# Kernel tuning notes

Hardware: AMD Instinct MI355X
Metric: run time of the kernel (lower is better)

## Reference

```python
import jax, jax.numpy as jnp
import numpy as np

B, T, E, H = 4, 2048, 1024, 16
HS = E // H
FF = 4 * E


def _layernorm(x, g, b, eps=1e-5):
    mu = jnp.mean(x, axis=-1, keepdims=True)
    var = jnp.var(x, axis=-1, keepdims=True)
    return (x - mu) * jax.lax.rsqrt(var + eps) * g + b


def setup_inputs() -> dict:
    key = jax.random.key(0)
    ks = jax.random.split(key, 12)
    s = E ** -0.5
    return {
        "x": jax.random.normal(ks[0], (B, T, E), jnp.float32),
        "Wq": jax.random.normal(ks[1], (E, E), jnp.float32) * s,
        "Wk": jax.random.normal(ks[2], (E, E), jnp.float32) * s,
        "Wv": jax.random.normal(ks[3], (E, E), jnp.float32) * s,
        "Wp": jax.random.normal(ks[4], (E, E), jnp.float32) * s,
        "bp": jnp.zeros((E,), jnp.float32),
        "W1": jax.random.normal(ks[5], (E, FF), jnp.float32) * s,
        "b1": jnp.zeros((FF,), jnp.float32),
        "W2": jax.random.normal(ks[6], (FF, E), jnp.float32) * (FF ** -0.5),
        "b2": jnp.zeros((E,), jnp.float32),
        "g1": jnp.ones((E,), jnp.float32),
        "be1": jnp.zeros((E,), jnp.float32),
        "g2": jnp.ones((E,), jnp.float32),
        "be2": jnp.zeros((E,), jnp.float32),
    }


def reference(x, Wq, Wk, Wv, Wp, bp, W1, b1, W2, b2, g1, be1, g2, be2):
    h = _layernorm(x, g1, be1)
    # per-head projections: Wq columns laid out head-by-head (matches concat order)
    q = (h @ Wq).reshape(B, T, H, HS).transpose(0, 2, 1, 3)  # [B,H,T,hs]
    k = (h @ Wk).reshape(B, T, H, HS).transpose(0, 2, 1, 3)
    v = (h @ Wv).reshape(B, T, H, HS).transpose(0, 2, 1, 3)
    # NOTE: original scales by full embedding size C**-0.5, not head_size
    scores = jnp.einsum("bhqd,bhkd->bhqk", q, k) * (E ** -0.5)
    causal = jnp.tril(jnp.ones((T, T), bool))
    scores = jnp.where(causal, scores, -jnp.inf)
    wei = jax.nn.softmax(scores, axis=-1)
    attn = jnp.einsum("bhqk,bhkd->bhqd", wei, v)  # [B,H,T,hs]
    attn = attn.transpose(0, 2, 1, 3).reshape(B, T, E)
    x = x + attn @ Wp + bp
    h2 = _layernorm(x, g2, be2)
    ff = jax.nn.relu(h2 @ W1 + b1) @ W2 + b2
    return x + ff
```

## Files before the change

kernel.cpp:

```cpp
#include <hip/hip_runtime.h>
#include <stdint.h>

typedef unsigned short u16;
typedef short s8v __attribute__((ext_vector_type(8)));
typedef float f32x4 __attribute__((ext_vector_type(4)));

#define B_SZ 4
#define T_SEQ 2048
#define E_DIM 1024
#define H_NUM 16
#define HS 64
#define FF_DIM 4096
#define M_ROWS 8192
#define QSCALE 0.0450842200f

__device__ __forceinline__ u16 f2bf(float f) {
    unsigned int u = __builtin_bit_cast(unsigned int, f);
    u += 0x7fffu + ((u >> 16) & 1u);
    return (u16)(u >> 16);
}

__device__ __forceinline__ float bf2f(u16 u) {
    unsigned int v = ((unsigned int)u) << 16;
    return __builtin_bit_cast(float, v);
}

__device__ __forceinline__ void async_copy16(const void* g, void* l) {
    __builtin_amdgcn_global_load_lds(
        (const __attribute__((address_space(1))) unsigned int*)g,
        (__attribute__((address_space(3))) unsigned int*)l, 16, 0, 0);
}

__global__ __launch_bounds__(256)
void transpose_cast4(const float* __restrict__ s0, const float* __restrict__ s1,
                     const float* __restrict__ s2, const float* __restrict__ s3,
                     u16* __restrict__ dqkv, u16* __restrict__ dp) {
    __shared__ float tile[32][33];
    const int zz = blockIdx.z;
    const float* src = (zz == 0) ? s0 : (zz == 1) ? s1 : (zz == 2) ? s2 : s3;
    u16* dst = (zz < 3) ? dqkv + (size_t)zz * 1048576 : dp;
    int n0 = blockIdx.x * 32, k0 = blockIdx.y * 32;
    int tx = threadIdx.x, ty = threadIdx.y;
#pragma unroll
    for (int i = 0; i < 4; i++)
        tile[ty + i * 8][tx] = src[(size_t)(k0 + ty + i * 8) * 1024 + n0 + tx];
    __syncthreads();
#pragma unroll
    for (int i = 0; i < 4; i++)
        dst[(size_t)(n0 + ty + i * 8) * 1024 + k0 + tx] = f2bf(tile[tx][ty + i * 8]);
}

__global__ __launch_bounds__(256)
void transpose_cast_w12(const float* __restrict__ W1, const float* __restrict__ W2,
                        u16* __restrict__ d1, u16* __restrict__ d2) {
    __shared__ float tile[32][33];
    const int zz = blockIdx.z;
    const float* src;
    u16* dst;
    int n0, k0, N, K;
    if (zz == 0) {
        src = W1; dst = d1; N = 4096; K = 1024;
        n0 = blockIdx.x * 32; k0 = blockIdx.y * 32;
    } else {
        src = W2; dst = d2; N = 1024; K = 4096;
        int idx = blockIdx.y * 128 + blockIdx.x;
        n0 = (idx & 31) * 32; k0 = (idx >> 5) * 32;
    }
    int tx = threadIdx.x, ty = threadIdx.y;
#pragma unroll
    for (int i = 0; i < 4; i++)
        tile[ty + i * 8][tx] = src[(size_t)(k0 + ty + i * 8) * N + n0 + tx];
    __syncthreads();
#pragma unroll
    for (int i = 0; i < 4; i++)
        dst[(size_t)(n0 + ty + i * 8) * K + k0 + tx] = f2bf(tile[tx][ty + i * 8]);
}

__global__ __launch_bounds__(256)
void transpose_v(const u16* __restrict__ V, u16* __restrict__ VT) {
    __shared__ u16 tile[64][80];
    const int t0 = blockIdx.x * 64;
    const size_t hoff = (size_t)blockIdx.y * (T_SEQ * HS);
    const int r = threadIdx.x >> 2, c0 = (threadIdx.x & 3) * 16;
    const u16* src = V + hoff + (size_t)(t0 + r) * HS + c0;
    *(s8v*)&tile[r][c0] = *(const s8v*)src;
    *(s8v*)&tile[r][c0 + 8] = *(const s8v*)(src + 8);
    __syncthreads();
    u16 tmp[16];
#pragma unroll
    for (int e = 0; e < 16; e++) tmp[e] = tile[c0 + e][r];
    u16* dst = VT + hoff + (size_t)r * T_SEQ + t0 + c0;
    *(s8v*)dst = *(const s8v*)&tmp[0];
    *(s8v*)(dst + 8) = *(const s8v*)&tmp[8];
}

__global__ __launch_bounds__(256)
void ln_kernel(const float* __restrict__ x, const float* __restrict__ g,
               const float* __restrict__ b, u16* __restrict__ out) {
    int row = blockIdx.x;
    int tid = threadIdx.x;
    float4 v = ((const float4*)(x + (size_t)row * E_DIM))[tid];
    float s = v.x + v.y + v.z + v.w;
    float sq = v.x * v.x + v.y * v.y + v.z * v.z + v.w * v.w;
#pragma unroll
    for (int off = 32; off; off >>= 1) {
        s += __shfl_xor(s, off);
        sq += __shfl_xor(sq, off);
    }
    __shared__ float sh[8];
    int w = tid >> 6, lane = tid & 63;
    if (lane == 0) { sh[w] = s; sh[4 + w] = sq; }
    __syncthreads();
    s = sh[0] + sh[1] + sh[2] + sh[3];
    sq = sh[4] + sh[5] + sh[6] + sh[7];
    float mu = s * (1.f / E_DIM);
    float var = sq * (1.f / E_DIM) - mu * mu;
    float rs = rsqrtf(var + 1e-5f);
    float4 gv = ((const float4*)g)[tid];
    float4 bv = ((const float4*)b)[tid];
    ushort4 o;
    o.x = f2bf((v.x - mu) * rs * gv.x + bv.x);
    o.y = f2bf((v.y - mu) * rs * gv.y + bv.y);
    o.z = f2bf((v.z - mu) * rs * gv.z + bv.z);
    o.w = f2bf((v.w - mu) * rs * gv.w + bv.w);
    ((ushort4*)(out + (size_t)row * E_DIM))[tid] = o;
}

__global__ __launch_bounds__(256)
void ln_kernel_bf(const u16* __restrict__ x, const float* __restrict__ g,
                  const float* __restrict__ b, u16* __restrict__ out) {
    int row = blockIdx.x;
    int tid = threadIdx.x;
    ushort4 uv = ((const ushort4*)(x + (size_t)row * E_DIM))[tid];
    float4 v;
    v.x = bf2f(uv.x); v.y = bf2f(uv.y); v.z = bf2f(uv.z); v.w = bf2f(uv.w);
    float s = v.x + v.y + v.z + v.w;
    float sq = v.x * v.x + v.y * v.y + v.z * v.z + v.w * v.w;
#pragma unroll
    for (int off = 32; off; off >>= 1) {
        s += __shfl_xor(s, off);
        sq += __shfl_xor(sq, off);
    }
    __shared__ float sh[8];
    int w = tid >> 6, lane = tid & 63;
    if (lane == 0) { sh[w] = s; sh[4 + w] = sq; }
    __syncthreads();
    s = sh[0] + sh[1] + sh[2] + sh[3];
    sq = sh[4] + sh[5] + sh[6] + sh[7];
    float mu = s * (1.f / E_DIM);
    float var = sq * (1.f / E_DIM) - mu * mu;
    float rs = rsqrtf(var + 1e-5f);
    float4 gv = ((const float4*)g)[tid];
    float4 bv = ((const float4*)b)[tid];
    ushort4 o;
    o.x = f2bf((v.x - mu) * rs * gv.x + bv.x);
    o.y = f2bf((v.y - mu) * rs * gv.y + bv.y);
    o.z = f2bf((v.z - mu) * rs * gv.z + bv.z);
    o.w = f2bf((v.w - mu) * rs * gv.w + bv.w);
    ((ushort4*)(out + (size_t)row * E_DIM))[tid] = o;
}

template <int MODE>
__global__ __launch_bounds__(512)
void gemm_bt128(const u16* __restrict__ A, const u16* __restrict__ BT,
                int M, int N, int K,
                const float* __restrict__ bias, const float* __restrict__ resid,
                float* __restrict__ outf, u16* __restrict__ outb) {
    __shared__ __align__(16) u16 As[3][256 * 64];
    __shared__ __align__(16) u16 Bs[3][128 * 64];

    const int gx = gridDim.x;
    const int nwg = gx * gridDim.y;
    const int l = blockIdx.y * gx + blockIdx.x;
    const int sw = (l & 7) * (nwg >> 3) + (l >> 3);
    const int tRow = (sw / gx) * 256, tCol = (sw % gx) * 128;

    const int tid = threadIdx.x, w = tid >> 6, lane = tid & 63;
    const int wr = w >> 1, wc = w & 1, lr = lane & 15, hg = lane >> 4;
    const int nk = K >> 6;

    f32x4 z = {0.f, 0.f, 0.f, 0.f};
    f32x4 acc[4][4];
#pragma unroll
    for (int m = 0; m < 4; m++)
#pragma unroll
        for (int n = 0; n < 4; n++) acc[m][n] = z;

    auto STAGE_A = [&](int kt, int c) {
#pragma unroll
        for (int i = 0; i < 4; i++) {
            int chunk = i * 512 + tid;
            int row = chunk >> 3, j = chunk & 7;
            int js = (j ^ (row & 7)) << 3;
            async_copy16(A + (size_t)(tRow + row) * K + (kt << 6) + js,
                         &As[c][(i * 512 + w * 64) * 8]);
        }
    };
    auto STAGE_B = [&](int kt, int c) {
#pragma unroll
        for (int i = 0; i < 2; i++) {
            int chunk = i * 512 + tid;
            int row = chunk >> 3, j = chunk & 7;
            int js = (j ^ (row & 7)) << 3;
            async_copy16(BT + (size_t)(tCol + row) * K + (kt << 6) + js,
                         &Bs[c][(i * 512 + w * 64) * 8]);
        }
    };

    STAGE_A(0, 0); STAGE_B(0, 0);
    STAGE_A(1, 1); STAGE_B(1, 1);
    asm volatile("s_waitcnt vmcnt(6)" ::: "memory");
    asm volatile("s_barrier" ::: "memory");

    for (int t = 0; t < nk; ++t) {
        const int bu = t % 3, nx = (t + 2) % 3;
        const u16* Ab = &As[bu][0];
        const u16* Bb = &Bs[bu][0];
        const bool more = (t + 2 < nk);

        s8v af0[2][2], bf[4][2];
#pragma unroll
        for (int m = 0; m < 2; m++)
#pragma unroll
            for (int kk = 0; kk < 2; kk++) {
                int r = wr * 64 + m * 16 + lr;
                af0[m][kk] = *(const s8v*)&Ab[r * 64 + (((kk * 4 + hg) ^ (r & 7)) << 3)];
            }
#pragma unroll
        for (int n = 0; n < 4; n++)
#pragma unroll
            for (int kk = 0; kk < 2; kk++) {
                int r = wc * 64 + n * 16 + lr;
                bf[n][kk] = *(const s8v*)&Bb[r * 64 + (((kk * 4 + hg) ^ (r & 7)) << 3)];
            }
        if (more) STAGE_A(t + 2, nx);
        asm volatile("s_barrier" ::: "memory");
        __builtin_amdgcn_s_setprio(1);
#pragma unroll
        for (int m = 0; m < 2; m++)
#pragma unroll
            for (int n = 0; n < 4; n++)
#pragma unroll
                for (int kk = 0; kk < 2; kk++)
                    acc[m][n] = __builtin_amdgcn_mfma_f32_16x16x32_bf16(
                        af0[m][kk], bf[n][kk], acc[m][n], 0, 0, 0);
        __builtin_amdgcn_s_setprio(0);
        asm volatile("s_barrier" ::: "memory");

        s8v af1[2][2];
#pragma unroll
        for (int m = 0; m < 2; m++)
#pragma unroll
            for (int kk = 0; kk < 2; kk++) {
                int r = wr * 64 + (m + 2) * 16 + lr;
                af1[m][kk] = *(const s8v*)&Ab[r * 64 + (((kk * 4 + hg) ^ (r & 7)) << 3)];
            }
        if (more) STAGE_B(t + 2, nx);
        asm volatile("s_barrier" ::: "memory");
        __builtin_amdgcn_s_setprio(1);
#pragma unroll
        for (int m = 0; m < 2; m++)
#pragma unroll
            for (int n = 0; n < 4; n++)
#pragma unroll
                for (int kk = 0; kk < 2; kk++)
                    acc[m + 2][n] = __builtin_amdgcn_mfma_f32_16x16x32_bf16(
                        af1[m][kk], bf[n][kk], acc[m + 2][n], 0, 0, 0);
        __builtin_amdgcn_s_setprio(0);
        if (more) asm volatile("s_waitcnt vmcnt(6)" ::: "memory");
        else      asm volatile("s_waitcnt vmcnt(0)" ::: "memory");
        asm volatile("s_barrier" ::: "memory");
    }

#pragma unroll
    for (int m = 0; m < 4; m++)
#pragma unroll
        for (int n = 0; n < 4; n++)
#pragma unroll
            for (int r = 0; r < 4; r++) {
                int row = tRow + wr * 64 + m * 16 + hg * 4 + r;
                int col = tCol + wc * 64 + n * 16 + lr;
                float v = acc[m][n][r];
                if (MODE == 0) {
                    int type = col >> 10, c2 = col & 1023;
                    int h = c2 >> 6, d = c2 & 63;
                    int bb = row >> 11, tt = row & 2047;
                    if (type == 0) v *= QSCALE;
                    outb[(size_t)type * 8388608 +
                         (((size_t)(bb * H_NUM + h) * T_SEQ + tt) << 6) + d] = f2bf(v);
                } else if (MODE == 1) {
                    v += bias[col];
                    v = fmaxf(v, 0.f);
                    outb[(size_t)row * N + col] = f2bf(v);
                } else {
                    outb[(size_t)row * N + col] =
                        f2bf(resid[(size_t)row * N + col] + v + bias[col]);
                }
            }
}

template <int MODE>
__global__ __launch_bounds__(512)
void gemm_bt256(const u16* __restrict__ A, const u16* __restrict__ BT,
                int M, int N, int Kst, int klen,
                const float* __restrict__ bias, const float* __restrict__ resid,
                float* __restrict__ outf, u16* __restrict__ outb) {
    __shared__ __align__(16) u16 As[2][256 * 64];
    __shared__ __align__(16) u16 Bs[2][256 * 64];

    const int gx = gridDim.x;
    const int nwg = gx * gridDim.y;
    const int l = blockIdx.y * gx + blockIdx.x;
    const int sw = (l & 7) * (nwg >> 3) + (l >> 3);
    const int tRow = (sw / gx) * 256, tCol = (sw % gx) * 256;
    const size_t koff = (size_t)blockIdx.z * klen;
    const u16* Az = A + koff;
    const u16* BTz = BT + koff;

    const int tid = threadIdx.x, w = tid >> 6, lane = tid & 63;
    const int wr = w >> 2, wc = w & 3, lr = lane & 15, hg = lane >> 4;
    const int nk = klen >> 6;

    f32x4 z = {0.f, 0.f, 0.f, 0.f};
    f32x4 acc[8][4];
#pragma unroll
    for (int m = 0; m < 8; m++)
#pragma unroll
        for (int n = 0; n < 4; n++) acc[m][n] = z;

    auto STAGE_A = [&](int kt, int c, int h) {
#pragma unroll
        for (int i = 0; i < 2; i++) {
            int chunk = h * 1024 + i * 512 + tid;
            int row = chunk >> 3, j = chunk & 7;
            int js = (j ^ (row & 7)) << 3;
            async_copy16(Az + (size_t)(tRow + row) * Kst + (kt << 6) + js,
                         &As[c][(h * 1024 + i * 512 + w * 64) * 8]);
        }
    };
    auto STAGE_B = [&](int kt, int c, int h) {
#pragma unroll
        for (int i = 0; i < 2; i++) {
            int chunk = h * 1024 + i * 512 + tid;
            int row = chunk >> 3, j = chunk & 7;
            int js = (j ^ (row & 7)) << 3;
            async_copy16(BTz + (size_t)(tCol + row) * Kst + (kt << 6) + js,
                         &Bs[c][(h * 1024 + i * 512 + w * 64) * 8]);
        }
    };

    STAGE_B(0, 0, 0); STAGE_B(0, 0, 1); STAGE_A(0, 0, 0); STAGE_A(0, 0, 1);
    STAGE_B(1, 1, 0); STAGE_B(1, 1, 1); STAGE_A(1, 1, 0); STAGE_A(1, 1, 1);
    asm volatile("s_waitcnt vmcnt(6)" ::: "memory");
    asm volatile("s_barrier" ::: "memory");

    for (int t = 0; t < nk; ++t) {
        const int cur = t & 1;
        const u16* Ab = &As[cur][0];
        const u16* Bb = &Bs[cur][0];
        const bool more = (t + 2 < nk);

        s8v bf[4][2];
#pragma unroll
        for (int p = 0; p < 4; p++) {
            s8v af[2][2];
#pragma unroll
            for (int mm = 0; mm < 2; mm++)
#pragma unroll
                for (int kk = 0; kk < 2; kk++) {
                    int r = (2 * p + mm) * 32 + wr * 16 + lr;
                    af[mm][kk] = *(const s8v*)&Ab[r * 64 + (((kk * 4 + hg) ^ (r & 7)) << 3)];
                }
            if (p == 0) {
#pragma unroll
                for (int n = 0; n < 4; n++)
#pragma unroll
                    for (int kk = 0; kk < 2; kk++) {
                        int r = n * 64 + wc * 16 + lr;
                        bf[n][kk] = *(const s8v*)&Bb[r * 64 + (((kk * 4 + hg) ^ (r & 7)) << 3)];
                    }
            }
            if (more) {
                if (p == 0) STAGE_B(t + 2, cur, 0);
                else if (p == 1) STAGE_B(t + 2, cur, 1);
                else if (p == 2) STAGE_A(t + 2, cur, 0);
                else STAGE_A(t + 2, cur, 1);
            }
            asm volatile("s_barrier" ::: "memory");
            __builtin_amdgcn_s_setprio(1);
#pragma unroll
            for (int mm = 0; mm < 2; mm++)
#pragma unroll
                for (int n = 0; n < 4; n++)
#pragma unroll
                    for (int kk = 0; kk < 2; kk++)
                        acc[2 * p + mm][n] = __builtin_amdgcn_mfma_f32_16x16x32_bf16(
                            af[mm][kk], bf[n][kk], acc[2 * p + mm][n], 0, 0, 0);
            __builtin_amdgcn_s_setprio(0);
            if (p == 3) {
                if (more) asm volatile("s_waitcnt vmcnt(6)" ::: "memory");
                else      asm volatile("s_waitcnt vmcnt(0)" ::: "memory");
            }
            asm volatile("s_barrier" ::: "memory");
        }
    }

    u16* outp = outb;
    if (MODE == 3 && blockIdx.z == 1) outp = (u16*)outf;
#pragma unroll
    for (int m = 0; m < 8; m++)
#pragma unroll
        for (int n = 0; n < 4; n++)
#pragma unroll
            for (int r = 0; r < 4; r++) {
                int row = tRow + m * 32 + wr * 16 + hg * 4 + r;
                int col = tCol + n * 64 + wc * 16 + lr;
                float v = acc[m][n][r];
                if (MODE == 1) {
                    v += bias[col];
                    v = fmaxf(v, 0.f);
                    outp[(size_t)row * N + col] = f2bf(v);
                } else {
                    outp[(size_t)row * N + col] = f2bf(v);
                }
            }
}

__global__ __launch_bounds__(256)
void reduce_w2(const u16* __restrict__ p0, const u16* __restrict__ p1,
               const u16* __restrict__ resid, const float* __restrict__ bias,
               float* __restrict__ out) {
    const int total = M_ROWS * E_DIM / 4;
    for (int i = blockIdx.x * 256 + threadIdx.x; i < total; i += gridDim.x * 256) {
        ushort4 rr = ((const ushort4*)resid)[i];
        float4 bb = ((const float4*)bias)[i & 255];
        ushort4 a = ((const ushort4*)p0)[i];
        ushort4 c = ((const ushort4*)p1)[i];
        float4 o;
        o.x = bf2f(a.x) + bf2f(c.x) + bf2f(rr.x) + bb.x;
        o.y = bf2f(a.y) + bf2f(c.y) + bf2f(rr.y) + bb.y;
        o.z = bf2f(a.z) + bf2f(c.z) + bf2f(rr.z) + bb.z;
        o.w = bf2f(a.w) + bf2f(c.w) + bf2f(rr.w) + bb.w;
        ((float4*)out)[i] = o;
    }
}

__global__ __launch_bounds__(512)
void attn_kernel(const u16* __restrict__ Q, const u16* __restrict__ K,
                 const u16* __restrict__ VT, u16* __restrict__ O) {
    __shared__ u16 Ks[2][64 * 64];
    __shared__ u16 Vs[2][64 * 64];
    __shared__ u16 Pl[8][16 * 64];
    const int bh = blockIdx.y;
    const u16* Qh = Q + (size_t)bh * T_SEQ * HS;
    const u16* Kh = K + (size_t)bh * T_SEQ * HS;
    const u16* VTh = VT + (size_t)bh * T_SEQ * HS;
    const int tid = threadIdx.x, w = tid >> 6, lane = tid & 63;
    const int lr = lane & 15, hg = lane >> 4;
    const int swz = (lr & 7) << 3;
    const int bb = bh >> 4, hh = bh & 15;
    const f32x4 z = {0.f, 0.f, 0.f, 0.f};

    for (int half = 0; half < 2; ++half) {
        const int qt = half ? (15 - blockIdx.x) : blockIdx.x;
        const int qb = qt * 128;
        const int nt = 2 * qt + 2;

        s8v qf[2];
        {
            const int qrow = qb + w * 16 + lr;
            qf[0] = *(const s8v*)(Qh + (size_t)qrow * HS + hg * 8);
            qf[1] = *(const s8v*)(Qh + (size_t)qrow * HS + 32 + hg * 8);
        }
        f32x4 o[4] = {z, z, z, z};
        float m_run[4] = {-1e30f, -1e30f, -1e30f, -1e30f};
        float l_part[4] = {0.f, 0.f, 0.f, 0.f};

        auto STAGE = [&](int t, int c) {
            int chunk = tid;
            int row = chunk >> 3, j = chunk & 7;
            int js = (j ^ (row & 7)) << 3;
            async_copy16(Kh + (size_t)t * (64 * HS) + row * HS + js, &Ks[c][w * 512]);
            async_copy16(VTh + (size_t)row * T_SEQ + t * 64 + js, &Vs[c][w * 512]);
        };

        int cur = 0;
        STAGE(0, 0);
        __syncthreads();

        for (int t = 0; t < nt; ++t) {
            if (t + 1 < nt) STAGE(t + 1, cur ^ 1);

            f32x4 s[4];
            __builtin_amdgcn_s_setprio(1);
#pragma unroll
            for (int n = 0; n < 4; n++) {
                f32x4 a = z;
#pragma unroll
                for (int kc = 0; kc < 2; kc++) {
                    s8v bfr = *(const s8v*)&Ks[cur][((n * 16 + lr) * 64 + kc * 32 + hg * 8) ^ swz];
                    a = __builtin_amdgcn_mfma_f32_16x16x32_bf16(qf[kc], bfr, a, 0, 0, 0);
                }
                s[n] = a;
            }
            __builtin_amdgcn_s_setprio(0);
            const bool diag = (t >= nt - 2);
            if (diag) {
#pragma unroll
                for (int n = 0; n < 4; n++)
#pragma unroll
                    for (int r = 0; r < 4; r++)
                        if ((t * 64 + n * 16 + lr) > (qb + w * 16 + hg * 4 + r))
                            s[n][r] = -1e30f;
            }
            float d0[4][4];
            float dm = -1e30f;
#pragma unroll
            for (int n = 0; n < 4; n++)
#pragma unroll
                for (int r = 0; r < 4; r++) {
                    d0[n][r] = s[n][r] - m_run[r];
                    dm = fmaxf(dm, d0[n][r]);
                }
            if (__any(dm > 8.f)) {
                float pm[4];
#pragma unroll
                for (int r = 0; r < 4; r++) {
                    float m0 = fmaxf(fmaxf(s[0][r], s[1][r]), fmaxf(s[2][r], s[3][r]));
                    m0 = fmaxf(m0, __shfl_xor(m0, 1));
                    m0 = fmaxf(m0, __shfl_xor(m0, 2));
                    m0 = fmaxf(m0, __shfl_xor(m0, 4));
                    m0 = fmaxf(m0, __shfl_xor(m0, 8));
                    pm[r] = m0;
                }
#pragma unroll
                for (int r = 0; r < 4; r++) {
                    float mn = fmaxf(m_run[r], pm[r]);
                    float al = __builtin_amdgcn_exp2f(m_run[r] - mn);
                    m_run[r] = mn;
                    l_part[r] *= al;
                    o[0][r] *= al; o[1][r] *= al; o[2][r] *= al; o[3][r] *= al;
                }
#pragma unroll
                for (int n = 0; n < 4; n++)
#pragma unroll
                    for (int r = 0; r < 4; r++) d0[n][r] = s[n][r] - m_run[r];
            }
#pragma unroll
            for (int n = 0; n < 4; n++)
#pragma unroll
                for (int r = 0; r < 4; r++) {
                    float p = __builtin_amdgcn_exp2f(d0[n][r]);
                    s[n][r] = p;
                    l_part[r] += p;
                }
            u16* Pw = &Pl[w][0];
#pragma unroll
            for (int n = 0; n < 4; n++)
#pragma unroll
                for (int r = 0; r < 4; r++) {
                    int prow = hg * 4 + r;
                    float pv = s[n][r];
                    Pw[(prow * 64 + n * 16 + lr) ^ ((prow & 7) << 3)] =
                        (u16)(__builtin_bit_cast(unsigned int, pv) >> 16);
                }
            asm volatile("s_waitcnt lgkmcnt(0)" ::: "memory");
            __builtin_amdgcn_s_setprio(1);
#pragma unroll
            for (int n = 0; n < 4; n++) {
#pragma unroll
                for (int kc = 0; kc < 2; kc++) {
                    s8v pa = *(const s8v*)&Pw[(lr * 64 + kc * 32 + hg * 8) ^ swz];
                    s8v vb = *(const s8v*)&Vs[cur][((n * 16 + lr) * 64 + kc * 32 + hg * 8) ^ swz];
                    o[n] = __builtin_amdgcn_mfma_f32_16x16x32_bf16(pa, vb, o[n], 0, 0, 0);
                }
            }
            __builtin_amdgcn_s_setprio(0);
            __syncthreads();
            cur ^= 1;
        }
        float rl[4];
#pragma unroll
        for (int r = 0; r < 4; r++) {
            float lsum = l_part[r];
            lsum += __shfl_xor(lsum, 1);
            lsum += __shfl_xor(lsum, 2);
            lsum += __shfl_xor(lsum, 4);
            lsum += __shfl_xor(lsum, 8);
            rl[r] = 1.f / lsum;
        }
#pragma unroll
        for (int n = 0; n < 4; n++)
#pragma unroll
            for (int r = 0; r < 4; r++) {
                int trow = qb + w * 16 + hg * 4 + r;
                O[((size_t)(bb * T_SEQ + trow)) * E_DIM + hh * HS + n * 16 + lr] =
                    f2bf(o[n][r] * rl[r]);
            }
    }
}

extern "C" void kernel_launch(void* const* d_in, const int* in_sizes, int n_in,
                              void* d_out, int out_size, void* d_ws, size_t ws_size,
                              hipStream_t stream) {
    (void)in_sizes; (void)n_in; (void)out_size; (void)ws_size;
    const float* x  = (const float*)d_in[0];
    const float* Wq = (const float*)d_in[1];
    const float* Wk = (const float*)d_in[2];
    const float* Wv = (const float*)d_in[3];
    const float* Wp = (const float*)d_in[4];
    const float* bp = (const float*)d_in[5];
    const float* W1 = (const float*)d_in[6];
    const float* b1 = (const float*)d_in[7];
    const float* W2 = (const float*)d_in[8];
    const float* b2 = (const float*)d_in[9];
    const float* g1  = (const float*)d_in[10];
    const float* be1 = (const float*)d_in[11];
    const float* g2  = (const float*)d_in[12];
    const float* be2 = (const float*)d_in[13];

    char* ws = (char*)d_ws;
    u16* wqkv_t  = (u16*)(ws);
    u16* wp_t    = (u16*)(ws + 6291456);
    u16* w1_t    = (u16*)(ws + 8388608);
    u16* w2_t    = (u16*)(ws + 16777216);
    u16* h_bf    = (u16*)(ws + 25165824);
    u16* q_bf    = (u16*)(ws + 41943040);
    u16* attn_bf = q_bf + 3 * 8388608;
    u16* ff1     = q_bf;
    u16* x2b     = (u16*)(ws + 109051904);
    u16* vt_bf   = h_bf;
    u16* part0   = (u16*)ws;
    u16* part1   = h_bf;

    dim3 b32(32, 8);
    transpose_cast4<<<dim3(32, 32, 4), b32, 0, stream>>>(Wq, Wk, Wv, Wp, wqkv_t, wp_t);
    transpose_cast_w12<<<dim3(128, 32, 2), b32, 0, stream>>>(W1, W2, w1_t, w2_t);

    ln_kernel<<<M_ROWS, 256, 0, stream>>>(x, g1, be1, h_bf);
    gemm_bt128<0><<<dim3(24, 32), 512, 0, stream>>>(h_bf, wqkv_t, M_ROWS, 3072, 1024,
                                                    nullptr, nullptr, nullptr, q_bf);
    transpose_v<<<dim3(32, 64), 256, 0, stream>>>(q_bf + 2 * 8388608, vt_bf);
    attn_kernel<<<dim3(8, 64), 512, 0, stream>>>(q_bf, q_bf + 8388608, vt_bf, attn_bf);
    gemm_bt128<2><<<dim3(8, 32), 512, 0, stream>>>(attn_bf, wp_t, M_ROWS, 1024, 1024,
                                                   bp, x, nullptr, x2b);
    ln_kernel_bf<<<M_ROWS, 256, 0, stream>>>(x2b, g2, be2, h_bf);
    gemm_bt256<1><<<dim3(16, 32), 512, 0, stream>>>(h_bf, w1_t, M_ROWS, 4096, 1024, 1024,
                                                    b1, nullptr, nullptr, ff1);
    gemm_bt256<3><<<dim3(4, 32, 2), 512, 0, stream>>>(ff1, w2_t, M_ROWS, 1024, 4096, 2048,
                                                      nullptr, nullptr, (float*)part1, part0);
    reduce_w2<<<2048, 256, 0, stream>>>(part0, part1, x2b, b2, (float*)d_out);
}
```

Before: 343.6 us.

## Software-pipeline LDS fragment reads with MFMA using double-buffered registers

Restructures the GEMM main loop so the A fragments for the next phase, and the A/B fragments for the next k-tile, are read from LDS while the current phase's MFMAs run. Two register sets alternate between phases, and the loop is unrolled by two so the B fragment buffers swap roles. This also removes one of the two barriers per phase. The goal is to hide LDS read latency behind matrix-core work and cut synchronisation, at the cost of more live registers. The unroll-by-two assumes an even tile count.

```diff
diff --git a/kernel.cpp b/kernel.cpp
--- a/kernel.cpp
+++ b/kernel.cpp
@@ -349,61 +349,83 @@
         }
     };
 
+    s8v afa[2][2], afb[2][2];
+    s8v bfa[4][2], bfb[4][2];
+
+    auto READ_A = [&](const u16* Ab, int p, s8v (&af)[2][2]) {
+#pragma unroll
+        for (int mm = 0; mm < 2; mm++)
+#pragma unroll
+            for (int kk = 0; kk < 2; kk++) {
+                int r = (2 * p + mm) * 32 + wr * 16 + lr;
+                af[mm][kk] = *(const s8v*)&Ab[r * 64 + (((kk * 4 + hg) ^ (r & 7)) << 3)];
+            }
+    };
+    auto READ_B = [&](const u16* Bb, s8v (&bf)[4][2]) {
+#pragma unroll
+        for (int n = 0; n < 4; n++)
+#pragma unroll
+            for (int kk = 0; kk < 2; kk++) {
+                int r = n * 64 + wc * 16 + lr;
+                bf[n][kk] = *(const s8v*)&Bb[r * 64 + (((kk * 4 + hg) ^ (r & 7)) << 3)];
+            }
+    };
+
     STAGE_B(0, 0, 0); STAGE_B(0, 0, 1); STAGE_A(0, 0, 0); STAGE_A(0, 0, 1);
     STAGE_B(1, 1, 0); STAGE_B(1, 1, 1); STAGE_A(1, 1, 0); STAGE_A(1, 1, 1);
     asm volatile("s_waitcnt vmcnt(6)" ::: "memory");
     asm volatile("s_barrier" ::: "memory");
-
-    for (int t = 0; t < nk; ++t) {
+    READ_A(&As[0][0], 0, afa);
+    READ_B(&Bs[0][0], bfa);
+
+#define MFMA8(AF, BF, R0)                                                      \
+    __builtin_amdgcn_s_setprio(1);                                             \
+    _Pragma("unroll") for (int mm = 0; mm < 2; mm++)                           \
+        _Pragma("unroll") for (int n = 0; n < 4; n++)                          \
+            _Pragma("unroll") for (int kk = 0; kk < 2; kk++)                   \
+                acc[R0 + mm][n] = __builtin_amdgcn_mfma_f32_16x16x32_bf16(     \
+                    AF[mm][kk], BF[n][kk], acc[R0 + mm][n], 0, 0, 0);          \
+    __builtin_amdgcn_s_setprio(0);
+
+    auto TILE = [&](int t, s8v (&bf)[4][2], s8v (&bfn)[4][2]) {
         const int cur = t & 1;
         const u16* Ab = &As[cur][0];
-        const u16* Bb = &Bs[cur][0];
-        const bool more = (t + 2 < nk);
-
-        s8v bf[4][2];
-#pragma unroll
-        for (int p = 0; p < 4; p++) {
-            s8v af[2][2];
-#pragma unroll
-            for (int mm = 0; mm < 2; mm++)
-#pragma unroll
-                for (int kk = 0; kk < 2; kk++) {
-                    int r = (2 * p + mm) * 32 + wr * 16 + lr;
-                    af[mm][kk] = *(const s8v*)&Ab[r * 64 + (((kk * 4 + hg) ^ (r & 7)) << 3)];
-                }
-            if (p == 0) {
-#pragma unroll
-                for (int n = 0; n < 4; n++)
-#pragma unroll
-                    for (int kk = 0; kk < 2; kk++) {
-                        int r = n * 64 + wc * 16 + lr;
-                        bf[n][kk] = *(const s8v*)&Bb[r * 64 + (((kk * 4 + hg) ^ (r & 7)) << 3)];
-                    }
-            }
-            if (more) {
-                if (p == 0) STAGE_B(t + 2, cur, 0);
-                else if (p == 1) STAGE_B(t + 2, cur, 1);
-                else if (p == 2) STAGE_A(t + 2, cur, 0);
-                else STAGE_A(t + 2, cur, 1);
-            }
-            asm volatile("s_barrier" ::: "memory");
-            __builtin_amdgcn_s_setprio(1);
-#pragma unroll
-            for (int mm = 0; mm < 2; mm++)
-#pragma unroll
-                for (int n = 0; n < 4; n++)
-#pragma unroll
-                    for (int kk = 0; kk < 2; kk++)
-                        acc[2 * p + mm][n] = __builtin_amdgcn_mfma_f32_16x16x32_bf16(
-                            af[mm][kk], bf[n][kk], acc[2 * p + mm][n], 0, 0, 0);
-            __builtin_amdgcn_s_setprio(0);
-            if (p == 3) {
-                if (more) asm volatile("s_waitcnt vmcnt(6)" ::: "memory");
-                else      asm volatile("s_waitcnt vmcnt(0)" ::: "memory");
-            }
-            asm volatile("s_barrier" ::: "memory");
-        }
+        const u16* AbN = &As[cur ^ 1][0];
+        const u16* BbN = &Bs[cur ^ 1][0];
+        const bool stage_more = (t + 2 < nk);
+        const bool read_more = (t + 1 < nk);
+
+        MFMA8(afa, bf, 0);
+        if (stage_more) STAGE_B(t + 2, cur, 0);
+        READ_A(Ab, 1, afb);
+        asm volatile("s_barrier" ::: "memory");
+
+        MFMA8(afb, bf, 2);
+        if (stage_more) STAGE_B(t + 2, cur, 1);
+        READ_A(Ab, 2, afa);
+        asm volatile("s_barrier" ::: "memory");
+
+        MFMA8(afa, bf, 4);
+        if (stage_more) STAGE_A(t + 2, cur, 0);
+        READ_A(Ab, 3, afb);
+        asm volatile("s_barrier" ::: "memory");
+
+        MFMA8(afb, bf, 6);
+        if (stage_more) asm volatile("s_waitcnt vmcnt(6)" ::: "memory");
+        else            asm volatile("s_waitcnt vmcnt(0)" ::: "memory");
+        if (stage_more) STAGE_A(t + 2, cur, 1);
+        if (read_more) {
+            READ_A(AbN, 0, afa);
+            READ_B(BbN, bfn);
+        }
+        asm volatile("s_barrier" ::: "memory");
+    };
+
+    for (int tt = 0; tt < nk; tt += 2) {
+        TILE(tt, bfa, bfb);
+        TILE(tt + 1, bfb, bfa);
     }
+#undef MFMA8
 
     u16* outp = outb;
     if (MODE == 3 && blockIdx.z == 1) outp = (u16*)outf;
```

New measurement: 400.9 us. +16.7%, slower.
